# Optimization experiments

Hardware: AMD Instinct MI355X
Metric: run time of the kernel (lower is better)

The kernel has to match this reference:

```python
import jax, jax.numpy as jnp
import numpy as np

DEPTH = 8           # perfect binary tree depth -> 255 branches, 256 leaves
B = 524288          # number of input rows
F = 32              # number of features
N_OUT = 8           # outputs per leaf


def _build_tree(depth):
    """Replicates BaseTree.__init__'s enumerate_tree on a perfect binary tree.
    Returns cond, cond_mask of shape [n_leaf, n_branch] (bool)."""
    n_nodes = 2 ** (depth + 1) - 1
    n_branch = 2 ** depth - 1  # heap order: nodes < n_branch are branches
    is_branch = np.zeros(n_nodes, dtype=bool)
    node_conditions = np.zeros((n_nodes, n_nodes), dtype=bool)
    node_conditions_mask = np.zeros((n_nodes, n_nodes), dtype=bool)

    def enumerate_tree(node_id, parent_id=None):
        if parent_id is not None:
            node_conditions_mask[node_id] = node_conditions_mask[parent_id]
            node_conditions_mask[node_id][parent_id] = True
        if node_id < n_branch:
            left_id, right_id = 2 * node_id + 1, 2 * node_id + 2
            is_branch[node_id] = True
            node_conditions[left_id] = node_conditions[node_id]
            node_conditions[right_id] = node_conditions[node_id]
            node_conditions[right_id][node_id] = True
            enumerate_tree(left_id, node_id)
            enumerate_tree(right_id, node_id)

    enumerate_tree(0)
    is_leaf = ~is_branch
    branch_ids = np.nonzero(is_branch)[0]
    leaf_ids = np.nonzero(is_leaf)[0]
    cond = node_conditions[np.ix_(leaf_ids, branch_ids)]
    cond_mask = node_conditions_mask[np.ix_(leaf_ids, branch_ids)]
    return cond, cond_mask


def setup_inputs() -> dict:
    key = jax.random.key(0)
    k_x, k_t, k_v = jax.random.split(key, 3)
    cond_np, cond_mask_np = _build_tree(DEPTH)
    n_branch = cond_np.shape[1]
    rng = np.random.default_rng(0)
    feature = jnp.asarray(rng.integers(0, F, size=n_branch), dtype=jnp.int32)
    x = jax.random.normal(k_x, (B, F), dtype=jnp.float32)
    threshold = jax.random.normal(k_t, (n_branch,), dtype=jnp.float32) * 0.5
    value = jax.random.normal(k_v, (cond_np.shape[0], N_OUT), dtype=jnp.float32)
    return {
        "x": x,
        "feature": feature,
        "threshold": threshold,
        "cond": jnp.asarray(cond_np),            # [n_leaf, n_branch] bool
        "cond_mask": jnp.asarray(cond_mask_np),  # [n_leaf, n_branch] bool
        "value": value,                            # [n_leaf, n_out]
    }


def reference(x, feature, threshold, cond, cond_mask, value):
    # comparisons: [B, n_branch] int8 (x[:, feature] > threshold)
    comp = (x[:, feature] > threshold[None, :]).astype(jnp.int8)
    c8 = cond.astype(jnp.int8)
    m8 = cond_mask.astype(jnp.int8)
    # [B, n_leaf] int32 counts via int8 matmuls (accumulate in int32)
    cond_counts = jnp.matmul(comp, c8.T, preferred_element_type=jnp.int32)
    mask_counts = jnp.matmul(comp, m8.T, preferred_element_type=jnp.int32)
    cond_sum = jnp.sum(c8.astype(jnp.int32), axis=1)  # [n_leaf]
    no_false_neg = cond_counts == cond_sum[None, :]
    no_false_pos = cond_counts == mask_counts
    leaf_idx = jnp.argmax((no_false_neg & no_false_pos).astype(jnp.int32), axis=-1)
    return value[leaf_idx]  # [B, n_out]
```

## Files before the change

### kernel.cpp

```cpp
#include <hip/hip_runtime.h>

#define N_ROWS 524288
#define F 32
#define NB 255
#define DEPTH 8
#define ROWS_PER_BLOCK 256
#define XSTRIDE 36

__global__ __launch_bounds__(256) void tree_traverse_kernel(
    const float* __restrict__ x,
    const int*   __restrict__ feature,
    const float* __restrict__ threshold,
    const float* __restrict__ value,
    float*       __restrict__ out)
{
    __shared__ float xs[ROWS_PER_BLOCK * XSTRIDE];
    __shared__ float s_thr[256];
    __shared__ int   s_feat[256];

    const int tid = threadIdx.x;
    const long long block_row0 = (long long)blockIdx.x * ROWS_PER_BLOCK;

    if (tid < NB) {
        s_feat[tid] = feature[tid];
        s_thr[tid]  = threshold[tid];
    }

    const float4* xg = reinterpret_cast<const float4*>(x + block_row0 * F);
    #pragma unroll
    for (int k = 0; k < 8; ++k) {
        int idx = tid + k * 256;
        float4 v = xg[idx];
        int row = idx >> 3;
        int f4  = idx & 7;
        *reinterpret_cast<float4*>(&xs[row * XSTRIDE + f4 * 4]) = v;
    }

    __syncthreads();

    const float* row_x = &xs[tid * XSTRIDE];
    int node = 0;
    #pragma unroll
    for (int d = 0; d < DEPTH; ++d) {
        int   f = s_feat[node];
        float t = s_thr[node];
        node = 2 * node + 1 + (row_x[f] > t ? 1 : 0);
    }
    const int leaf = node - NB;

    const float4* v4 = reinterpret_cast<const float4*>(value + (size_t)leaf * 8);
    float4 v0 = v4[0];
    float4 v1 = v4[1];
    float4* o = reinterpret_cast<float4*>(out + (block_row0 + tid) * 8);
    o[0] = v0;
    o[1] = v1;
}

extern "C" void kernel_launch(void* const* d_in, const int* in_sizes, int n_in,
                              void* d_out, int out_size, void* d_ws, size_t ws_size,
                              hipStream_t stream) {
    (void)in_sizes; (void)n_in; (void)d_ws; (void)ws_size; (void)out_size;
    const float* x         = (const float*)d_in[0];
    const int*   feature   = (const int*)d_in[1];
    const float* threshold = (const float*)d_in[2];
    const float* value     = (const float*)d_in[5];
    float*       out       = (float*)d_out;

    dim3 grid(N_ROWS / ROWS_PER_BLOCK);
    dim3 block(256);
    tree_traverse_kernel<<<grid, block, 0, stream>>>(x, feature, threshold, value, out);
}
```

Measured before the change: 18.98 us.

## Make tree traversal wave-local, drop block barrier, prefetch two row chunks

```diff
diff --git a/kernel.cpp b/kernel.cpp
--- a/kernel.cpp
+++ b/kernel.cpp
@@ -1,59 +1,74 @@
 #include <hip/hip_runtime.h>
 
-#define N_ROWS 524288
-#define F 32
 #define NB 255
 #define DEPTH 8
-#define ROWS_PER_BLOCK 256
+#define F 32
 #define XSTRIDE 36
+#define ROWS_PER_WAVE 64
+#define CHUNKS 2
+#define WAVES 4
+#define N_ROWS 524288
 
-__global__ __launch_bounds__(256) void tree_traverse_kernel(
+__global__ __launch_bounds__(256) void tree_traverse_pipelined(
     const float* __restrict__ x,
     const int*   __restrict__ feature,
     const float* __restrict__ threshold,
     const float* __restrict__ value,
     float*       __restrict__ out)
 {
-    __shared__ float xs[ROWS_PER_BLOCK * XSTRIDE];
-    __shared__ float s_thr[256];
-    __shared__ int   s_feat[256];
+    __shared__ float xs[WAVES][ROWS_PER_WAVE * XSTRIDE];
+    __shared__ int2  s_node[256];
 
-    const int tid = threadIdx.x;
-    const long long block_row0 = (long long)blockIdx.x * ROWS_PER_BLOCK;
+    const int tid  = threadIdx.x;
+    const int lane = tid & 63;
+    const int wid  = tid >> 6;
 
-    if (tid < NB) {
-        s_feat[tid] = feature[tid];
-        s_thr[tid]  = threshold[tid];
+    #pragma unroll
+    for (int k = 0; k < 4; ++k) {
+        int e = lane + 64 * k;
+        if (e < NB) s_node[e] = make_int2(feature[e], __float_as_int(threshold[e]));
     }
 
-    const float4* xg = reinterpret_cast<const float4*>(x + block_row0 * F);
+    const int       gwave = blockIdx.x * WAVES + wid;
+    const long long row0  = (long long)gwave * (ROWS_PER_WAVE * CHUNKS);
+    const float4*   xg    = reinterpret_cast<const float4*>(x + row0 * F);
+
+    float4 A[8], B[8];
     #pragma unroll
-    for (int k = 0; k < 8; ++k) {
-        int idx = tid + k * 256;
-        float4 v = xg[idx];
-        int row = idx >> 3;
-        int f4  = idx & 7;
-        *reinterpret_cast<float4*>(&xs[row * XSTRIDE + f4 * 4]) = v;
+    for (int j = 0; j < 8; ++j) A[j] = xg[j * 64 + lane];
+    #pragma unroll
+    for (int j = 0; j < 8; ++j) B[j] = xg[512 + j * 64 + lane];
+
+    float* myxs = xs[wid];
+    const float* row_x = &myxs[lane * XSTRIDE];
+
+    #pragma unroll
+    for (int c = 0; c < CHUNKS; ++c) {
+        #pragma unroll
+        for (int j = 0; j < 8; ++j) {
+            float4 v = (c == 0) ? A[j] : B[j];
+            int f4idx = j * 64 + lane;
+            int row   = f4idx >> 3;
+            int cc    = f4idx & 7;
+            *reinterpret_cast<float4*>(&myxs[row * XSTRIDE + cc * 4]) = v;
+        }
+
+        int node = 0;
+        #pragma unroll
+        for (int d = 0; d < DEPTH; ++d) {
+            int2  nd = s_node[node];
+            float t  = __int_as_float(nd.y);
+            node = 2 * node + 1 + (row_x[nd.x] > t ? 1 : 0);
+        }
+        const int leaf = node - NB;
+
+        const float4* v4 = reinterpret_cast<const float4*>(value + (size_t)leaf * 8);
+        float4 v0 = v4[0];
+        float4 v1 = v4[1];
+        float4* o = reinterpret_cast<float4*>(out + (row0 + c * ROWS_PER_WAVE + lane) * 8);
+        o[0] = v0;
+        o[1] = v1;
     }
-
-    __syncthreads();
-
-    const float* row_x = &xs[tid * XSTRIDE];
-    int node = 0;
-    #pragma unroll
-    for (int d = 0; d < DEPTH; ++d) {
-        int   f = s_feat[node];
-        float t = s_thr[node];
-        node = 2 * node + 1 + (row_x[f] > t ? 1 : 0);
-    }
-    const int leaf = node - NB;
-
-    const float4* v4 = reinterpret_cast<const float4*>(value + (size_t)leaf * 8);
-    float4 v0 = v4[0];
-    float4 v1 = v4[1];
-    float4* o = reinterpret_cast<float4*>(out + (block_row0 + tid) * 8);
-    o[0] = v0;
-    o[1] = v1;
 }
 
 extern "C" void kernel_launch(void* const* d_in, const int* in_sizes, int n_in,
@@ -66,7 +81,7 @@
     const float* value     = (const float*)d_in[5];
     float*       out       = (float*)d_out;
 
-    dim3 grid(N_ROWS / ROWS_PER_BLOCK);
+    dim3 grid(N_ROWS / (ROWS_PER_WAVE * CHUNKS * WAVES));
     dim3 block(256);
-    tree_traverse_kernel<<<grid, block, 0, stream>>>(x, feature, threshold, value, out);
+    tree_traverse_pipelined<<<grid, block, 0, stream>>>(x, feature, threshold, value, out);
 }
```

Result: slower. 19.47 us (+2.6%).
